# Kernel optimization log

Measured on AMD Instinct MI355X. Metric: run time of the kernel, lower is better.

## Reference

```python
import jax, jax.numpy as jnp
import numpy as np

B, N, D, DEG = 16, 8192, 384, 16
K, H, STEPS = 8, 128, 3


def setup_inputs() -> dict:
    key = jax.random.key(0)
    ks = jax.random.split(key, 8)
    s_in = 1.0 / np.sqrt(2 * D)
    s_h = 1.0 / np.sqrt(H)
    return {
        "q_embs": jax.random.normal(ks[0], (B, D), jnp.float32),
        "emb": jax.random.normal(ks[1], (B, N, D), jnp.float32),
        "neighbors": jax.random.randint(ks[2], (B, N, DEG), 0, N, jnp.int32),
        "labels": jax.random.randint(ks[3], (B, N), 0, 2, jnp.int32),
        "W1": jax.random.normal(ks[4], (2 * D, H), jnp.float32) * s_in,
        "b1": jnp.zeros((H,), jnp.float32),
        "W2": jax.random.normal(ks[5], (H, K), jnp.float32) * s_h,
        "b2": jnp.zeros((K,), jnp.float32),
        "P1": jax.random.normal(ks[6], (2 * D, H), jnp.float32) * s_in,
        "pb1": jnp.zeros((H,), jnp.float32),
        "P2": jax.random.normal(ks[7], (H, 1), jnp.float32) * s_h,
        "pb2": jnp.zeros((1,), jnp.float32),
    }


def reference(q_embs, emb, neighbors, labels, W1, b1, W2, b2, P1, pb1, P2, pb2):
    b, n, d = emb.shape
    k = W2.shape[1]
    # inp = [emb | q broadcast]  -> [B, N, 2D]
    inp = jnp.concatenate([emb, jnp.broadcast_to(q_embs[:, None, :], emb.shape)], axis=-1)
    # path_net: sigmoid(MLP) -> [B, N], then +1 at support (label==1) nodes
    path = jax.nn.sigmoid(jax.nn.relu(inp @ P1 + pb1) @ P2 + pb2)[..., 0]
    path = path + labels.astype(path.dtype)
    # coin_net amplitudes scaled by (1 + path)
    amps = (jax.nn.relu(inp @ W1 + b1) @ W2 + b2) * (1.0 + path)[..., None]  # [B,N,K]
    # initial uniform state
    state = jnp.full((b, n, k), 1.0 / np.sqrt(n * k), dtype=emb.dtype)

    # sparse adjacency diffusion: out[i] = sum_{j in nbrs[i]} st[j]
    spmm = jax.vmap(lambda st, nb: st[nb].sum(axis=1))  # st [N,K], nb [N,DEG]

    for _ in range(STEPS):
        st = spmm(state * amps, neighbors)                 # [B,N,K]
        norm = jnp.linalg.norm(st.reshape(b, -1), axis=1)[:, None, None]
        state = jnp.where(norm > 0, st / norm, st)
    return jnp.abs(state).sum(axis=-1)  # [B,N]
```

## Files before the change

kernel.cpp:

```cpp
#include <hip/hip_runtime.h>
#include <cstdint>
#include <cstddef>

#define BB 16
#define NN 8192
#define DD 384
#define HH 128
#define KK 8
#define DEG 16

typedef short bf8_t __attribute__((ext_vector_type(8)));
typedef float f4_t __attribute__((ext_vector_type(4)));

typedef const __attribute__((address_space(1))) unsigned char* gcp_t;
typedef __attribute__((address_space(3))) unsigned char* lcp_t;

__device__ __forceinline__ void glds16(const void* g, void* l) {
  __builtin_amdgcn_global_load_lds((gcp_t)g, (lcp_t)l, 16, 0, 0);
}

__device__ __forceinline__ unsigned short f2bf(float f) {
  unsigned int u = __float_as_uint(f);
  u += 0x7FFFu + ((u >> 16) & 1u);
  return (unsigned short)(u >> 16);
}

__device__ __forceinline__ bf8_t pack8(float4 f0, float4 f1) {
  union { unsigned short us[8]; bf8_t v; } pk;
  pk.us[0] = f2bf(f0.x); pk.us[1] = f2bf(f0.y);
  pk.us[2] = f2bf(f0.z); pk.us[3] = f2bf(f0.w);
  pk.us[4] = f2bf(f1.x); pk.us[5] = f2bf(f1.y);
  pk.us[6] = f2bf(f1.z); pk.us[7] = f2bf(f1.w);
  return pk.v;
}

__global__ __launch_bounds__(256) void kprep(
    const float* __restrict__ q, const float* __restrict__ W1,
    const float* __restrict__ b1, const float* __restrict__ P1,
    const float* __restrict__ pb1,
    unsigned short* __restrict__ W1t, unsigned short* __restrict__ P1t,
    float* __restrict__ base1, float* __restrict__ baseP,
    float* __restrict__ normsq)
{
  int blk = blockIdx.x, t = threadIdx.x;
  if (blk < 32) {
    int b = blk >> 1, net = blk & 1;
    const float* W = (net ? P1 : W1) + (size_t)DD * HH;
    const float* qb = q + b * DD;
    int h = t & 127, half = t >> 7;
    int d0 = half * 192;
    float a0 = 0.f, a1 = 0.f, a2 = 0.f, a3 = 0.f;
    for (int d = d0; d < d0 + 192; d += 4) {
      a0 = fmaf(qb[d],     W[(size_t)d * HH + h],       a0);
      a1 = fmaf(qb[d + 1], W[(size_t)(d + 1) * HH + h], a1);
      a2 = fmaf(qb[d + 2], W[(size_t)(d + 2) * HH + h], a2);
      a3 = fmaf(qb[d + 3], W[(size_t)(d + 3) * HH + h], a3);
    }
    __shared__ float red[256];
    red[t] = (a0 + a1) + (a2 + a3);
    __syncthreads();
    if (t < 128) {
      float tot = red[t] + red[t + 128] + (net ? pb1[h] : b1[h]);
      (net ? baseP : base1)[b * HH + h] = tot;
    }
  } else {
    int e = (blk - 32) * 3072 + t;
    for (int it = 0; it < 12; ++it, e += 256) {
      int net = e / 49152;
      int r = e - net * 49152;
      int d = r >> 7;
      int h = r & 127;
      float v = (net ? P1 : W1)[d * HH + h];
      int ph = d >> 6;
      int rem = d & 63;
      int cb = rem >> 3, wi = rem & 7;
      int c = cb ^ (h & 7);
      (net ? P1t : W1t)[ph * 8192 + h * 64 + c * 8 + wi] = f2bf(v);
    }
    if (blk == 32 && t < BB) normsq[t] = 0.f;
  }
}

__global__ __launch_bounds__(512, 4) void kgemm(
    const float* __restrict__ emb,
    const unsigned short* __restrict__ W1t, const unsigned short* __restrict__ P1t,
    const float* __restrict__ base1, const float* __restrict__ baseP,
    const float* __restrict__ W2, const float* __restrict__ b2,
    const float* __restrict__ P2, const float* __restrict__ pb2,
    float* __restrict__ rawamps, float* __restrict__ pslogit)
{
  __shared__ __align__(16) unsigned short sB[2][128 * 64];
  __shared__ float sW2a[128 * 9];
  __shared__ float sBase[128];
  __shared__ float sP2[128];
  __shared__ float sB2[8];

  const int g = blockIdx.x;
  const int slot = g & 7;
  const int net = (g >> 3) & 1;
  const int wid = (g >> 4) * 8 + slot;
  const int b = wid >> 5;
  const int rowbase = (wid & 31) * 256;

  const int t = threadIdx.x;
  const int w = t >> 6, lane = t & 63, q = lane >> 4, ln = lane & 15;
  const int fl = ln & 7;

  const unsigned short* Wsw = net ? P1t : W1t;

  {
    const unsigned short* src = Wsw + w * 512 + lane * 8;
    char* dst = (char*)&sB[0][0] + w * 1024;
    glds16(src,        dst);
    glds16(src + 4096, dst + 8192);
  }
  if (t < 128) sBase[t] = (net ? baseP : base1)[b * HH + t];
  if (net == 0) {
    for (int e = t; e < HH * KK; e += 512) {
      int h = e >> 3, kk = e & 7;
      sW2a[h * 9 + kk] = W2[e];
    }
    if (t < 8) sB2[t] = b2[t];
  } else if (t >= 128 && t < 256) {
    sP2[t - 128] = P2[t - 128];
  }

  const float* ar0 = emb + (size_t)(b * NN + rowbase + w * 32 + ln) * DD + q * 8;
  const float* ar1 = ar0 + (size_t)16 * DD;
  float4 pf[4];
  pf[0] = ((const float4*)ar0)[0]; pf[1] = ((const float4*)ar0)[1];
  pf[2] = ((const float4*)ar1)[0]; pf[3] = ((const float4*)ar1)[1];

  f4_t acc[2][8];
  f4_t zero = {0.f, 0.f, 0.f, 0.f};
#pragma unroll
  for (int i = 0; i < 8; ++i) { acc[0][i] = zero; acc[1][i] = zero; }

  __syncthreads();

#pragma unroll
  for (int ph = 0; ph < 6; ++ph) {
    if (ph < 5) {
      const unsigned short* src = Wsw + (ph + 1) * 8192 + w * 512 + lane * 8;
      char* dst = (char*)&sB[0][0] + ((ph + 1) & 1) * 16384 + w * 1024;
      glds16(src,        dst);
      glds16(src + 4096, dst + 8192);
    }
    const char* bbase = (const char*)&sB[0][0] + (ph & 1) * 16384;
#pragma unroll
    for (int jl = 0; jl < 2; ++jl) {
      const int j = ph * 2 + jl;
      bf8_t af0 = pack8(pf[0], pf[1]);
      bf8_t af1 = pack8(pf[2], pf[3]);
      if (j + 1 < 12) {
        const float* p0 = ar0 + (j + 1) * 32;
        const float* p1 = ar1 + (j + 1) * 32;
        pf[0] = ((const float4*)p0)[0]; pf[1] = ((const float4*)p0)[1];
        pf[2] = ((const float4*)p1)[0]; pf[3] = ((const float4*)p1)[1];
      }
      const int cb = jl * 4 + q;
#pragma unroll
      for (int ct = 0; ct < 8; ++ct) {
        const int h = ct * 16 + ln;
        bf8_t bf = *(const bf8_t*)(bbase + h * 128 + ((cb ^ fl) << 4));
        acc[0][ct] = __builtin_amdgcn_mfma_f32_16x16x32_bf16(af0, bf, acc[0][ct], 0, 0, 0);
        acc[1][ct] = __builtin_amdgcn_mfma_f32_16x16x32_bf16(af1, bf, acc[1][ct], 0, 0, 0);
      }
    }
    if (ph < 5) __syncthreads();
  }

  const float pb2v = pb2[0];
#pragma unroll
  for (int grp = 0; grp < 2; ++grp) {
#pragma unroll
    for (int r = 0; r < 4; ++r) {
      const int grow = rowbase + w * 32 + grp * 16 + q * 4 + r;
      if (net == 0) {
        float s[8];
#pragma unroll
        for (int kk = 0; kk < 8; ++kk) s[kk] = 0.f;
#pragma unroll
        for (int ct = 0; ct < 8; ++ct) {
          int col = ct * 16 + ln;
          float h1 = fmaxf(acc[grp][ct][r] + sBase[col], 0.f);
#pragma unroll
          for (int kk = 0; kk < 8; ++kk) s[kk] = fmaf(h1, sW2a[col * 9 + kk], s[kk]);
        }
#pragma unroll
        for (int off = 1; off < 16; off <<= 1)
#pragma unroll
          for (int kk = 0; kk < 8; ++kk) s[kk] += __shfl_xor(s[kk], off, 64);
        if (ln == 0) {
          float4 o0, o1;
          o0.x = s[0] + sB2[0]; o0.y = s[1] + sB2[1];
          o0.z = s[2] + sB2[2]; o0.w = s[3] + sB2[3];
          o1.x = s[4] + sB2[4]; o1.y = s[5] + sB2[5];
          o1.z = s[6] + sB2[6]; o1.w = s[7] + sB2[7];
          float4* dst = (float4*)(rawamps + (size_t)(b * NN + grow) * KK);
          dst[0] = o0; dst[1] = o1;
        }
      } else {
        float ps = 0.f;
#pragma unroll
        for (int ct = 0; ct < 8; ++ct) {
          int col = ct * 16 + ln;
          float hp = fmaxf(acc[grp][ct][r] + sBase[col], 0.f);
          ps = fmaf(hp, sP2[col], ps);
        }
#pragma unroll
        for (int off = 1; off < 16; off <<= 1) ps += __shfl_xor(ps, off, 64);
        if (ln == 0) pslogit[b * NN + grow] = ps + pb2v;
      }
    }
  }
}

__global__ __launch_bounds__(256) void applyscale(
    const float* __restrict__ raw, const float* __restrict__ psl,
    const int* __restrict__ lab, float* __restrict__ ampsS)
{
  int node = blockIdx.x * 256 + threadIdx.x;
  float sc = 1.f + 1.f / (1.f + __expf(-psl[node])) + (float)lab[node];
  const float4* r = (const float4*)(raw + (size_t)node * KK);
  float4 v0 = r[0], v1 = r[1];
  v0.x *= sc; v0.y *= sc; v0.z *= sc; v0.w *= sc;
  v1.x *= sc; v1.y *= sc; v1.z *= sc; v1.w *= sc;
  float4* d = (float4*)(ampsS + (size_t)node * KK);
  d[0] = v0; d[1] = v1;
}

template<bool MUL, bool NRM>
__global__ __launch_bounds__(256) void sgl2(
    const int* __restrict__ nbr, const float* __restrict__ src,
    const float* __restrict__ mult, float* __restrict__ out,
    float* __restrict__ normsq)
{
  const int g = blockIdx.x;
  const int b = ((g & 7) << 1) | ((g >> 3) & 1);
  const int chunk = g >> 4;
  const int t = threadIdx.x;
  const int n = chunk * 256 + t;
  const size_t node = (size_t)b * NN + n;

  const int4* nbp = (const int4*)(nbr + node * DEG);
  int4 q0 = nbp[0], q1 = nbp[1], q2 = nbp[2], q3 = nbp[3];

  const f4_t* sp = (const f4_t*)(src + (size_t)b * NN * KK);
  f4_t a0 = {0.f, 0.f, 0.f, 0.f}, a1 = {0.f, 0.f, 0.f, 0.f};

#define GATHER(idx) { const f4_t* p = sp + (((size_t)(unsigned)(idx)) << 1); \
                      a0 += p[0]; a1 += p[1]; }
  GATHER(q0.x) GATHER(q0.y) GATHER(q0.z) GATHER(q0.w)
  GATHER(q1.x) GATHER(q1.y) GATHER(q1.z) GATHER(q1.w)
  GATHER(q2.x) GATHER(q2.y) GATHER(q2.z) GATHER(q2.w)
  GATHER(q3.x) GATHER(q3.y) GATHER(q3.z) GATHER(q3.w)
#undef GATHER

  if (MUL) {
    const f4_t* mp = (const f4_t*)(mult + node * KK);
    a0 *= mp[0]; a1 *= mp[1];
  }
  f4_t* op = (f4_t*)(out + node * KK);
  op[0] = a0; op[1] = a1;

  if (NRM) {
    float ss = a0[0]*a0[0] + a0[1]*a0[1] + a0[2]*a0[2] + a0[3]*a0[3]
             + a1[0]*a1[0] + a1[1]*a1[1] + a1[2]*a1[2] + a1[3]*a1[3];
#pragma unroll
    for (int o = 1; o < 64; o <<= 1) ss += __shfl_xor(ss, o, 64);
    if ((t & 63) == 0) atomicAdd(&normsq[b], ss);
  }
}

__global__ __launch_bounds__(256) void fout(
    const float* __restrict__ u, const float* __restrict__ normsq,
    float* __restrict__ out)
{
  int node = blockIdx.x * 256 + threadIdx.x;
  float ns = normsq[node >> 13];
  float inv = ns > 0.f ? rsqrtf(ns) : 1.f;
  const float4* p = (const float4*)(u + (size_t)node * KK);
  float4 v0 = p[0], v1 = p[1];
  out[node] = (fabsf(v0.x) + fabsf(v0.y) + fabsf(v0.z) + fabsf(v0.w) +
               fabsf(v1.x) + fabsf(v1.y) + fabsf(v1.z) + fabsf(v1.w)) * inv;
}

extern "C" void kernel_launch(void* const* d_in, const int* in_sizes, int n_in,
                              void* d_out, int out_size, void* d_ws, size_t ws_size,
                              hipStream_t stream) {
  const float* q   = (const float*)d_in[0];
  const float* emb = (const float*)d_in[1];
  const int*   nbr = (const int*)d_in[2];
  const int*   lab = (const int*)d_in[3];
  const float* W1  = (const float*)d_in[4];
  const float* b1  = (const float*)d_in[5];
  const float* W2  = (const float*)d_in[6];
  const float* b2  = (const float*)d_in[7];
  const float* P1  = (const float*)d_in[8];
  const float* pb1 = (const float*)d_in[9];
  const float* P2  = (const float*)d_in[10];
  const float* pb2 = (const float*)d_in[11];
  float* out = (float*)d_out;

  const size_t NK = (size_t)BB * NN * KK;
  float* ws     = (float*)d_ws;
  float* buf0   = ws;
  float* buf1   = buf0 + NK;
  float* buf2   = buf1 + NK;
  float* psl    = buf2 + NK;
  float* base1  = psl + (size_t)BB * NN;
  float* baseP  = base1 + BB * HH;
  float* normsq = baseP + BB * HH;
  unsigned short* W1t = (unsigned short*)(normsq + 16);
  unsigned short* P1t = W1t + (size_t)HH * DD;

  kprep<<<64, 256, 0, stream>>>(q, W1, b1, P1, pb1, W1t, P1t, base1, baseP, normsq);
  kgemm<<<1024, 512, 0, stream>>>(emb, W1t, P1t, base1, baseP, W2, b2, P2, pb2,
                                  buf0, psl);
  applyscale<<<512, 256, 0, stream>>>(buf0, psl, lab, buf1);
  sgl2<true,  false><<<512, 256, 0, stream>>>(nbr, buf1, buf1, buf2, normsq);
  sgl2<true,  false><<<512, 256, 0, stream>>>(nbr, buf2, buf1, buf0, normsq);
  sgl2<false, true ><<<512, 256, 0, stream>>>(nbr, buf0, buf0, buf2, normsq);
  fout<<<512, 256, 0, stream>>>(buf2, normsq, out);
}
```

Measured before the change: 407.1 us.

## Fuse three diffusion steps into one LDS-resident kernel per batch-channel plane

Switches amplitudes to a channel-planar layout and runs all three sparse diffusion steps in a single kernel where each block holds one (batch, channel) plane of amplitudes and state in shared memory. Gathers then read LDS instead of random global rows, and two kernel launches plus intermediate global round-trips are removed. In exchange only 128 large blocks run, and each block rereads the batch's neighbor lists every step, multiplying neighbor-index traffic by the channel count.

```diff
diff --git a/kernel.cpp b/kernel.cpp
--- a/kernel.cpp
+++ b/kernel.cpp
@@ -218,72 +218,97 @@
 
 __global__ __launch_bounds__(256) void applyscale(
     const float* __restrict__ raw, const float* __restrict__ psl,
-    const int* __restrict__ lab, float* __restrict__ ampsS)
+    const int* __restrict__ lab, float* __restrict__ ampsP)
 {
   int node = blockIdx.x * 256 + threadIdx.x;
   float sc = 1.f + 1.f / (1.f + __expf(-psl[node])) + (float)lab[node];
   const float4* r = (const float4*)(raw + (size_t)node * KK);
   float4 v0 = r[0], v1 = r[1];
-  v0.x *= sc; v0.y *= sc; v0.z *= sc; v0.w *= sc;
-  v1.x *= sc; v1.y *= sc; v1.z *= sc; v1.w *= sc;
-  float4* d = (float4*)(ampsS + (size_t)node * KK);
-  d[0] = v0; d[1] = v1;
-}
-
-template<bool MUL, bool NRM>
-__global__ __launch_bounds__(256) void sgl2(
-    const int* __restrict__ nbr, const float* __restrict__ src,
-    const float* __restrict__ mult, float* __restrict__ out,
-    float* __restrict__ normsq)
-{
+  const int BN = BB * NN;
+  ampsP[0 * BN + node] = v0.x * sc;
+  ampsP[1 * BN + node] = v0.y * sc;
+  ampsP[2 * BN + node] = v0.z * sc;
+  ampsP[3 * BN + node] = v0.w * sc;
+  ampsP[4 * BN + node] = v1.x * sc;
+  ampsP[5 * BN + node] = v1.y * sc;
+  ampsP[6 * BN + node] = v1.z * sc;
+  ampsP[7 * BN + node] = v1.w * sc;
+}
+
+__global__ __launch_bounds__(1024, 4) void sdiff(
+    const int* __restrict__ nbr, const float* __restrict__ ampsP,
+    float* __restrict__ u3P, float* __restrict__ normsq)
+{
+  __shared__ float sAmp[NN];
+  __shared__ float sSt[NN];
   const int g = blockIdx.x;
-  const int b = ((g & 7) << 1) | ((g >> 3) & 1);
-  const int chunk = g >> 4;
+  const int b = g >> 3;
+  const int k = g & 7;
   const int t = threadIdx.x;
-  const int n = chunk * 256 + t;
-  const size_t node = (size_t)b * NN + n;
-
-  const int4* nbp = (const int4*)(nbr + node * DEG);
-  int4 q0 = nbp[0], q1 = nbp[1], q2 = nbp[2], q3 = nbp[3];
-
-  const f4_t* sp = (const f4_t*)(src + (size_t)b * NN * KK);
-  f4_t a0 = {0.f, 0.f, 0.f, 0.f}, a1 = {0.f, 0.f, 0.f, 0.f};
-
-#define GATHER(idx) { const f4_t* p = sp + (((size_t)(unsigned)(idx)) << 1); \
-                      a0 += p[0]; a1 += p[1]; }
-  GATHER(q0.x) GATHER(q0.y) GATHER(q0.z) GATHER(q0.w)
-  GATHER(q1.x) GATHER(q1.y) GATHER(q1.z) GATHER(q1.w)
-  GATHER(q2.x) GATHER(q2.y) GATHER(q2.z) GATHER(q2.w)
-  GATHER(q3.x) GATHER(q3.y) GATHER(q3.z) GATHER(q3.w)
-#undef GATHER
-
-  if (MUL) {
-    const f4_t* mp = (const f4_t*)(mult + node * KK);
-    a0 *= mp[0]; a1 *= mp[1];
-  }
-  f4_t* op = (f4_t*)(out + node * KK);
-  op[0] = a0; op[1] = a1;
-
-  if (NRM) {
-    float ss = a0[0]*a0[0] + a0[1]*a0[1] + a0[2]*a0[2] + a0[3]*a0[3]
-             + a1[0]*a1[0] + a1[1]*a1[1] + a1[2]*a1[2] + a1[3]*a1[3];
-#pragma unroll
-    for (int o = 1; o < 64; o <<= 1) ss += __shfl_xor(ss, o, 64);
-    if ((t & 63) == 0) atomicAdd(&normsq[b], ss);
-  }
+  const int BN = BB * NN;
+
+  {
+    const float4* p4 = (const float4*)(ampsP + (size_t)k * BN + (size_t)b * NN);
+    float4* s4 = (float4*)sAmp;
+    s4[t] = p4[t];
+    s4[t + 1024] = p4[t + 1024];
+  }
+  const int* nbase = nbr + (size_t)b * NN * DEG;
+  __syncthreads();
+
+  float res[8];
+
+#define GSTEP(SRC)                                                         \
+  _Pragma("unroll")                                                        \
+  for (int i = 0; i < 8; ++i) {                                            \
+    const int n = i * 1024 + t;                                            \
+    const int4* np = (const int4*)(nbase + (size_t)n * DEG);               \
+    int4 q0 = np[0], q1 = np[1], q2 = np[2], q3 = np[3];                   \
+    float a = SRC[q0.x] + SRC[q0.y] + SRC[q0.z] + SRC[q0.w]                \
+            + SRC[q1.x] + SRC[q1.y] + SRC[q1.z] + SRC[q1.w]                \
+            + SRC[q2.x] + SRC[q2.y] + SRC[q2.z] + SRC[q2.w]                \
+            + SRC[q3.x] + SRC[q3.y] + SRC[q3.z] + SRC[q3.w];               \
+    res[i] = a;                                                            \
+  }
+
+  GSTEP(sAmp)
+#pragma unroll
+  for (int i = 0; i < 8; ++i) sSt[i * 1024 + t] = res[i] * sAmp[i * 1024 + t];
+  __syncthreads();
+
+  GSTEP(sSt)
+  __syncthreads();
+#pragma unroll
+  for (int i = 0; i < 8; ++i) sSt[i * 1024 + t] = res[i] * sAmp[i * 1024 + t];
+  __syncthreads();
+
+  GSTEP(sSt)
+#undef GSTEP
+  float* oplane = u3P + (size_t)k * BN + (size_t)b * NN;
+  float ss = 0.f;
+#pragma unroll
+  for (int i = 0; i < 8; ++i) {
+    oplane[i * 1024 + t] = res[i];
+    ss = fmaf(res[i], res[i], ss);
+  }
+#pragma unroll
+  for (int o = 1; o < 64; o <<= 1) ss += __shfl_xor(ss, o, 64);
+  if ((t & 63) == 0) atomicAdd(&normsq[b], ss);
 }
 
 __global__ __launch_bounds__(256) void fout(
-    const float* __restrict__ u, const float* __restrict__ normsq,
+    const float* __restrict__ u3P, const float* __restrict__ normsq,
     float* __restrict__ out)
 {
   int node = blockIdx.x * 256 + threadIdx.x;
   float ns = normsq[node >> 13];
   float inv = ns > 0.f ? rsqrtf(ns) : 1.f;
-  const float4* p = (const float4*)(u + (size_t)node * KK);
-  float4 v0 = p[0], v1 = p[1];
-  out[node] = (fabsf(v0.x) + fabsf(v0.y) + fabsf(v0.z) + fabsf(v0.w) +
-               fabsf(v1.x) + fabsf(v1.y) + fabsf(v1.z) + fabsf(v1.w)) * inv;
+  const int BN = BB * NN;
+  float s = fabsf(u3P[0 * BN + node]) + fabsf(u3P[1 * BN + node])
+          + fabsf(u3P[2 * BN + node]) + fabsf(u3P[3 * BN + node])
+          + fabsf(u3P[4 * BN + node]) + fabsf(u3P[5 * BN + node])
+          + fabsf(u3P[6 * BN + node]) + fabsf(u3P[7 * BN + node]);
+  out[node] = s * inv;
 }
 
 extern "C" void kernel_launch(void* const* d_in, const int* in_sizes, int n_in,
@@ -319,8 +344,6 @@
   kgemm<<<1024, 512, 0, stream>>>(emb, W1t, P1t, base1, baseP, W2, b2, P2, pb2,
                                   buf0, psl);
   applyscale<<<512, 256, 0, stream>>>(buf0, psl, lab, buf1);
-  sgl2<true,  false><<<512, 256, 0, stream>>>(nbr, buf1, buf1, buf2, normsq);
-  sgl2<true,  false><<<512, 256, 0, stream>>>(nbr, buf2, buf1, buf0, normsq);
-  sgl2<false, true ><<<512, 256, 0, stream>>>(nbr, buf0, buf0, buf2, normsq);
+  sdiff<<<128, 1024, 0, stream>>>(nbr, buf1, buf2, normsq);
   fout<<<512, 256, 0, stream>>>(buf2, normsq, out);
 }
```

Result: slower. 456.3 us (+12.1%).
